# Kernel optimization log

Measured on AMD Instinct MI355X. Metric: run time of the kernel, lower is better.

Reference implementation:

```python
import jax, jax.numpy as jnp
import numpy as np

N = 100000
E = 1600000
D_IN = 128
D_H = 128
D_OUT = 128
LN_EPS = 1e-5
NORM_EPS = 1e-12


def _sage_conv(x, src, dst, Wl, bl, Wr):
    # PyG SAGEConv(mean): out = lin_l(mean_{j in N(i)} x_j) + lin_r(x_i)
    msgs = x[src]                                             # [E, d] gather
    summed = jax.ops.segment_sum(msgs, dst, num_segments=N)   # [N, d]
    cnt = jax.ops.segment_sum(jnp.ones((src.shape[0],), x.dtype), dst, num_segments=N)
    mean = summed / jnp.maximum(cnt, 1.0)[:, None]
    return mean @ Wl + bl + x @ Wr


def _layer_norm(x, g, b):
    mu = jnp.mean(x, axis=-1, keepdims=True)
    var = jnp.mean(jnp.square(x - mu), axis=-1, keepdims=True)
    return (x - mu) * jax.lax.rsqrt(var + LN_EPS) * g + b


def setup_inputs() -> dict:
    key = jax.random.key(0)
    ks = jax.random.split(key, 20)
    x = jax.random.normal(ks[0], (N, D_IN), dtype=jnp.float32)
    edge_index = jax.random.randint(ks[1], (2, E), 0, N, dtype=jnp.int64)
    dims = [(D_IN, D_H), (D_H, D_H), (D_H, D_OUT)]
    inp = {"x": x, "edge_index": edge_index}
    for i, (di, do) in enumerate(dims):
        s = 1.0 / np.sqrt(di)
        inp[f"Wl{i}"] = jax.random.normal(ks[2 + 5 * i], (di, do), dtype=jnp.float32) * s
        inp[f"bl{i}"] = jnp.zeros((do,), dtype=jnp.float32)
        inp[f"Wr{i}"] = jax.random.normal(ks[3 + 5 * i], (di, do), dtype=jnp.float32) * s
        inp[f"g{i}"] = jnp.ones((do,), dtype=jnp.float32)
        inp[f"b{i}"] = jnp.zeros((do,), dtype=jnp.float32)
    return inp


def reference(x, edge_index, Wl0, bl0, Wr0, g0, b0, Wl1, bl1, Wr1, g1, b1, Wl2, bl2, Wr2, g2, b2):
    src, dst = edge_index[0], edge_index[1]
    params = [(Wl0, bl0, Wr0, g0, b0), (Wl1, bl1, Wr1, g1, b1), (Wl2, bl2, Wr2, g2, b2)]
    h = x
    for i, (Wl, bl, Wr, g, b) in enumerate(params):
        h = _sage_conv(h, src, dst, Wl, bl, Wr)
        h = _layer_norm(h, g, b)
        if i < len(params) - 1:
            h = jax.nn.elu(h)
            # dropout is identity in eval mode
    # F.normalize(p=2, dim=-1)
    nrm = jnp.sqrt(jnp.sum(jnp.square(h), axis=-1, keepdims=True))
    return h / jnp.maximum(nrm, NORM_EPS)
```

## Files before the change

### kernel.cpp

```cpp
#include <hip/hip_runtime.h>
#include <hip/hip_bf16.h>
#include <math.h>

#define N_NODES 100000
#define N_EDGES 1600000
#define D 128
#define NB 391
#define BSTRIDE 6000

#define OFF_SSRC 0
#define OFF_OFFS 6400000
#define OFF_PACK 6800016
#define OFF_GC   7193232
#define OFF_BB   7195296
#define OFF_M    7204112
#define OFF_XHI  58404112
#define OFF_XLO  84004112

typedef __attribute__((ext_vector_type(8))) short short8;
typedef __attribute__((ext_vector_type(4))) float floatx4;

__device__ __forceinline__ unsigned short f2bf(float f) {
    unsigned int u = __float_as_uint(f);
    u += 0x7fffu + ((u >> 16) & 1u);
    return (unsigned short)(u >> 16);
}
__device__ __forceinline__ float bf2f(unsigned short h) {
    return __uint_as_float(((unsigned int)h) << 16);
}

__global__ __launch_bounds__(256) void part_kernel(const int* __restrict__ src,
                                                   const int* __restrict__ dst,
                                                   int* __restrict__ gcur,
                                                   uint2* __restrict__ staging) {
    __shared__ int hist[NB];
    __shared__ int base[NB];
    int t = threadIdx.x;
    int e0 = blockIdx.x * 4096;
    for (int i = t; i < NB; i += 256) hist[i] = 0;
    __syncthreads();
    int d[16];
#pragma unroll
    for (int i = 0; i < 16; ++i) {
        int e = e0 + i * 256 + t;
        d[i] = (e < N_EDGES) ? dst[e] : -1;
        if (d[i] >= 0) atomicAdd(&hist[d[i] >> 8], 1);
    }
    __syncthreads();
    for (int i = t; i < NB; i += 256) {
        int h = hist[i];
        base[i] = h ? atomicAdd(&gcur[i], h) : 0;
    }
    __syncthreads();
    for (int i = t; i < NB; i += 256) hist[i] = 0;
    __syncthreads();
#pragma unroll
    for (int i = 0; i < 16; ++i) {
        if (d[i] >= 0) {
            int e = e0 + i * 256 + t;
            int b = d[i] >> 8;
            int slot = atomicAdd(&hist[b], 1);
            staging[b * BSTRIDE + base[b] + slot] =
                make_uint2((unsigned)src[e], (unsigned)(d[i] & 255));
        }
    }
}

__global__ void bscan_kernel(const int* __restrict__ gcur, int* __restrict__ bbase,
                             int* __restrict__ offs) {
    __shared__ int sh[512];
    int t = threadIdx.x;
    int v = (t < NB) ? gcur[t] : 0;
    sh[t] = v;
    __syncthreads();
    for (int off = 1; off < 512; off <<= 1) {
        int y = (t >= off) ? sh[t - off] : 0;
        __syncthreads();
        sh[t] += y;
        __syncthreads();
    }
    if (t < NB) bbase[t] = sh[t] - v;
    if (t == 0) offs[N_NODES] = N_EDGES;
}

__global__ __launch_bounds__(256) void bsort_kernel(const uint2* __restrict__ staging,
                                                    const int* __restrict__ gcur,
                                                    const int* __restrict__ bbase,
                                                    int* __restrict__ offs,
                                                    int* __restrict__ s_src) {
    __shared__ int cnt[256];
    __shared__ int scn[256];
    __shared__ int ssrc[BSTRIDE];
    int b = blockIdx.x;
    int t = threadIdx.x;
    int n = gcur[b];
    int base_out = bbase[b];
    cnt[t] = 0;
    __syncthreads();
    for (int e = t; e < n; e += 256) {
        uint2 v = staging[b * BSTRIDE + e];
        atomicAdd(&cnt[v.y], 1);
    }
    __syncthreads();
    int v = cnt[t];
    scn[t] = v;
    __syncthreads();
    for (int off = 1; off < 256; off <<= 1) {
        int y = (t >= off) ? scn[t - off] : 0;
        __syncthreads();
        scn[t] += y;
        __syncthreads();
    }
    int ex = scn[t] - v;
    int node = b * 256 + t;
    if (node < N_NODES) offs[node] = base_out + ex;
    cnt[t] = ex;
    __syncthreads();
    for (int e = t; e < n; e += 256) {
        uint2 w = staging[b * BSTRIDE + e];
        int slot = atomicAdd(&cnt[w.y], 1);
        ssrc[slot] = (int)w.x;
    }
    __syncthreads();
    for (int e = t; e < n; e += 256) s_src[base_out + e] = ssrc[e];
}

__global__ void pack_kernel(const float* __restrict__ Wl0, const float* __restrict__ Wr0,
                            const float* __restrict__ Wl1, const float* __restrict__ Wr1,
                            const float* __restrict__ Wl2, const float* __restrict__ Wr2,
                            unsigned short* __restrict__ pack) {
    int tid = blockIdx.x * blockDim.x + threadIdx.x;
    int l = tid >> 15;
    int r = tid & 32767;
    int k = r >> 7;
    int n = r & 127;
    const float* Wl = (l == 0) ? Wl0 : (l == 1) ? Wl1 : Wl2;
    const float* Wr = (l == 0) ? Wr0 : (l == 1) ? Wr1 : Wr2;
    float v = (k < 128) ? Wl[k * 128 + n] : Wr[(k - 128) * 128 + n];
    unsigned short hi = f2bf(v);
    unsigned short lo = f2bf(v - bf2f(hi));
    int ct = n >> 4, ks = k >> 5, lane = ((k >> 3) & 3) * 16 + (n & 15), j = k & 7;
    int idx = ((ct * 8 + ks) * 64 + lane) * 8 + j;
    pack[l * 65536 + idx] = hi;
    pack[l * 65536 + 32768 + idx] = lo;
}

__global__ __launch_bounds__(256) void cvt_kernel(const float* __restrict__ x,
                                                  unsigned int* __restrict__ Xhi,
                                                  unsigned int* __restrict__ Xlo) {
    int i = blockIdx.x * 256 + threadIdx.x;
    float2 v = ((const float2*)x)[i];
    unsigned short h0 = f2bf(v.x), h1 = f2bf(v.y);
    unsigned short l0 = f2bf(v.x - bf2f(h0)), l1 = f2bf(v.y - bf2f(h1));
    Xhi[i] = (unsigned int)h0 | ((unsigned int)h1 << 16);
    Xlo[i] = (unsigned int)l0 | ((unsigned int)l1 << 16);
}

__global__ __launch_bounds__(256) void agg_kernel(const uint4* __restrict__ X4,
                                                  const int* __restrict__ s_src,
                                                  const int* __restrict__ offs,
                                                  float* __restrict__ mean) {
    int wid = threadIdx.x >> 6, lane = threadIdx.x & 63;
    int node = blockIdx.x * 4 + wid;
    int sub = lane >> 4, li = lane & 15;
    int beg = offs[node], end = offs[node + 1];
    int deg = end - beg;
    float acc[8];
#pragma unroll
    for (int j = 0; j < 8; ++j) acc[j] = 0.f;

#define ACC_U4(u)                                                                  \
    do {                                                                           \
        const unsigned int w_[4] = {(u).x, (u).y, (u).z, (u).w};                   \
        _Pragma("unroll") for (int j_ = 0; j_ < 4; ++j_) {                         \
            acc[2 * j_]     += bf2f((unsigned short)w_[j_]);                       \
            acc[2 * j_ + 1] += bf2f((unsigned short)(w_[j_] >> 16));               \
        }                                                                          \
    } while (0)

    for (int cbase = 0; cbase < deg; cbase += 64) {
        int cnt = min(deg - cbase, 64);
        int myidx = s_src[min(beg + cbase + lane, N_EDGES - 1)];
        int j = 0;
        for (; j + 16 <= cnt; j += 16) {
            int i0 = __shfl(myidx, j + sub);
            int i1 = __shfl(myidx, j + 4 + sub);
            int i2 = __shfl(myidx, j + 8 + sub);
            int i3 = __shfl(myidx, j + 12 + sub);
            uint4 u0 = X4[i0 * 16 + li];
            uint4 u1 = X4[i1 * 16 + li];
            uint4 u2 = X4[i2 * 16 + li];
            uint4 u3 = X4[i3 * 16 + li];
            ACC_U4(u0);
            ACC_U4(u1);
            ACC_U4(u2);
            ACC_U4(u3);
        }
        if (j + 8 <= cnt) {
            int i0 = __shfl(myidx, j + sub);
            int i1 = __shfl(myidx, j + 4 + sub);
            uint4 u0 = X4[i0 * 16 + li];
            uint4 u1 = X4[i1 * 16 + li];
            ACC_U4(u0);
            ACC_U4(u1);
            j += 8;
        }
        if (j + 4 <= cnt) {
            int i0 = __shfl(myidx, j + sub);
            uint4 u0 = X4[i0 * 16 + li];
            ACC_U4(u0);
            j += 4;
        }
        int rem = cnt - j;
        if (rem > 0) {
            int i0 = __shfl(myidx, j + min(sub, rem - 1));
            uint4 u0 = X4[i0 * 16 + li];
            if (sub < rem) ACC_U4(u0);
        }
    }
#undef ACC_U4

#pragma unroll
    for (int j = 0; j < 8; ++j) {
        acc[j] += __shfl_xor(acc[j], 16);
        acc[j] += __shfl_xor(acc[j], 32);
    }
    float inv = 1.0f / fmaxf((float)deg, 1.0f);
    if (sub < 2) {
        float4 v = make_float4(acc[sub * 4] * inv, acc[sub * 4 + 1] * inv,
                               acc[sub * 4 + 2] * inv, acc[sub * 4 + 3] * inv);
        *(float4*)&mean[node * D + li * 8 + sub * 4] = v;
    }
}

__global__ __launch_bounds__(256) void mmln_kernel(unsigned short* Xh,
                                                   unsigned short* Xl,
                                                   const float* __restrict__ mean,
                                                   const unsigned short* __restrict__ packh,
                                                   const unsigned short* __restrict__ packl,
                                                   const float* __restrict__ bl,
                                                   const float* __restrict__ g,
                                                   const float* __restrict__ b,
                                                   float* __restrict__ outf, int last) {
    int t = threadIdx.x;
    int lane = t & 63;
    int wid = t >> 6;
    int colb = lane & 15;
    int quad = lane >> 4;
    int kq = quad * 8;
    int tilebase = blockIdx.x * 128 + wid * 32;

    int rowA[2];
    rowA[0] = min(tilebase + colb, N_NODES - 1);
    rowA[1] = min(tilebase + 16 + colb, N_NODES - 1);

    floatx4 acc[2][8];
#pragma unroll
    for (int rt = 0; rt < 2; ++rt)
#pragma unroll
        for (int ct = 0; ct < 8; ++ct) acc[rt][ct] = (floatx4){0.f, 0.f, 0.f, 0.f};

#pragma unroll
    for (int ks = 0; ks < 4; ++ks) {
        int kof = ks * 32 + kq;
        short8 ah[2], al[2];
#pragma unroll
        for (int rt = 0; rt < 2; ++rt) {
            const float* p = mean + (long)rowA[rt] * D + kof;
            float4 v0 = *(const float4*)p;
            float4 v1 = *(const float4*)(p + 4);
            float v[8] = {v0.x, v0.y, v0.z, v0.w, v1.x, v1.y, v1.z, v1.w};
#pragma unroll
            for (int j = 0; j < 8; ++j) {
                unsigned short hi = f2bf(v[j]);
                ah[rt][j] = (short)hi;
                al[rt][j] = (short)f2bf(v[j] - bf2f(hi));
            }
        }
#pragma unroll
        for (int ct = 0; ct < 8; ++ct) {
            int fo = ((ct * 8 + ks) << 9) + (lane << 3);
            short8 bh = *(const short8*)(packh + fo);
            short8 bo = *(const short8*)(packl + fo);
#pragma unroll
            for (int rt = 0; rt < 2; ++rt) {
                acc[rt][ct] = __builtin_amdgcn_mfma_f32_16x16x32_bf16(ah[rt], bh, acc[rt][ct], 0, 0, 0);
                acc[rt][ct] = __builtin_amdgcn_mfma_f32_16x16x32_bf16(al[rt], bh, acc[rt][ct], 0, 0, 0);
                acc[rt][ct] = __builtin_amdgcn_mfma_f32_16x16x32_bf16(ah[rt], bo, acc[rt][ct], 0, 0, 0);
            }
        }
    }
#pragma unroll
    for (int ks = 4; ks < 8; ++ks) {
        int kof = (ks - 4) * 32 + kq;
        short8 ah[2], al[2];
#pragma unroll
        for (int rt = 0; rt < 2; ++rt) {
            long o = (long)rowA[rt] * D + kof;
            ah[rt] = *(const short8*)(Xh + o);
            al[rt] = *(const short8*)(Xl + o);
        }
#pragma unroll
        for (int ct = 0; ct < 8; ++ct) {
            int fo = ((ct * 8 + ks) << 9) + (lane << 3);
            short8 bh = *(const short8*)(packh + fo);
            short8 bo = *(const short8*)(packl + fo);
#pragma unroll
            for (int rt = 0; rt < 2; ++rt) {
                acc[rt][ct] = __builtin_amdgcn_mfma_f32_16x16x32_bf16(ah[rt], bh, acc[rt][ct], 0, 0, 0);
                acc[rt][ct] = __builtin_amdgcn_mfma_f32_16x16x32_bf16(al[rt], bh, acc[rt][ct], 0, 0, 0);
                acc[rt][ct] = __builtin_amdgcn_mfma_f32_16x16x32_bf16(ah[rt], bo, acc[rt][ct], 0, 0, 0);
            }
        }
    }

    float bb[8], gg[8], b2[8];
#pragma unroll
    for (int ct = 0; ct < 8; ++ct) {
        bb[ct] = bl[ct * 16 + colb];
        gg[ct] = g[ct * 16 + colb];
        b2[ct] = b[ct * 16 + colb];
    }

#pragma unroll
    for (int rt = 0; rt < 2; ++rt) {
#pragma unroll
        for (int ct = 0; ct < 8; ++ct)
#pragma unroll
            for (int e = 0; e < 4; ++e) acc[rt][ct][e] += bb[ct];
        float mu[4], rstd[4];
#pragma unroll
        for (int e = 0; e < 4; ++e) {
            float s = 0.f;
#pragma unroll
            for (int ct = 0; ct < 8; ++ct) s += acc[rt][ct][e];
            s += __shfl_xor(s, 1); s += __shfl_xor(s, 2);
            s += __shfl_xor(s, 4); s += __shfl_xor(s, 8);
            mu[e] = s * (1.0f / 128.0f);
        }
#pragma unroll
        for (int e = 0; e < 4; ++e) {
            float q = 0.f;
#pragma unroll
            for (int ct = 0; ct < 8; ++ct) {
                float d = acc[rt][ct][e] - mu[e];
                q += d * d;
            }
            q += __shfl_xor(q, 1); q += __shfl_xor(q, 2);
            q += __shfl_xor(q, 4); q += __shfl_xor(q, 8);
            rstd[e] = rsqrtf(q * (1.0f / 128.0f) + 1e-5f);
        }
#pragma unroll
        for (int ct = 0; ct < 8; ++ct)
#pragma unroll
            for (int e = 0; e < 4; ++e) {
                float y = (acc[rt][ct][e] - mu[e]) * rstd[e] * gg[ct] + b2[ct];
                if (!last) y = (y > 0.f) ? y : expm1f(y);
                acc[rt][ct][e] = y;
            }
        if (last) {
#pragma unroll
            for (int e = 0; e < 4; ++e) {
                float ss = 0.f;
#pragma unroll
                for (int ct = 0; ct < 8; ++ct) {
                    float y = acc[rt][ct][e];
                    ss += y * y;
                }
                ss += __shfl_xor(ss, 1); ss += __shfl_xor(ss, 2);
                ss += __shfl_xor(ss, 4); ss += __shfl_xor(ss, 8);
                float inv = 1.0f / fmaxf(sqrtf(ss), 1e-12f);
#pragma unroll
                for (int ct = 0; ct < 8; ++ct) acc[rt][ct][e] *= inv;
            }
#pragma unroll
            for (int e = 0; e < 4; ++e) {
                int row = tilebase + rt * 16 + quad * 4 + e;
                if (row < N_NODES) {
#pragma unroll
                    for (int ct = 0; ct < 8; ++ct)
                        outf[(long)row * D + ct * 16 + colb] = acc[rt][ct][e];
                }
            }
        } else {
#pragma unroll
            for (int e = 0; e < 4; ++e) {
                int row = tilebase + rt * 16 + quad * 4 + e;
                if (row < N_NODES) {
#pragma unroll
                    for (int ct = 0; ct < 8; ++ct) {
                        float y = acc[rt][ct][e];
                        unsigned short hh = f2bf(y);
                        unsigned short ll = f2bf(y - bf2f(hh));
                        long o = (long)row * D + ct * 16 + colb;
                        Xh[o] = hh;
                        Xl[o] = ll;
                    }
                }
            }
        }
    }
}

extern "C" void kernel_launch(void* const* d_in, const int* in_sizes, int n_in,
                              void* d_out, int out_size, void* d_ws, size_t ws_size,
                              hipStream_t stream) {
    const float* x = (const float*)d_in[0];
    const int* edges = (const int*)d_in[1];
    const int* src = edges;
    const int* dst = edges + N_EDGES;
    const float* Wl[3] = {(const float*)d_in[2], (const float*)d_in[7],  (const float*)d_in[12]};
    const float* bl[3] = {(const float*)d_in[3], (const float*)d_in[8],  (const float*)d_in[13]};
    const float* Wr[3] = {(const float*)d_in[4], (const float*)d_in[9],  (const float*)d_in[14]};
    const float* g[3]  = {(const float*)d_in[5], (const float*)d_in[10], (const float*)d_in[15]};
    const float* b[3]  = {(const float*)d_in[6], (const float*)d_in[11], (const float*)d_in[16]};

    char* ws = (char*)d_ws;
    int* s_src = (int*)(ws + OFF_SSRC);
    int* offs  = (int*)(ws + OFF_OFFS);
    unsigned short* wpack = (unsigned short*)(ws + OFF_PACK);
    int* gcur  = (int*)(ws + OFF_GC);
    int* bbase = (int*)(ws + OFF_BB);
    float* M = (float*)(ws + OFF_M);
    uint2* staging = (uint2*)(ws + OFF_M);
    unsigned short* Xhi = (unsigned short*)(ws + OFF_XHI);
    unsigned short* Xlo = (unsigned short*)(ws + OFF_XLO);
    float* out = (float*)d_out;

    hipMemsetAsync(gcur, 0, NB * sizeof(int), stream);
    part_kernel<<<(N_EDGES + 4095) / 4096, 256, 0, stream>>>(src, dst, gcur, staging);
    bscan_kernel<<<1, 512, 0, stream>>>(gcur, bbase, offs);
    bsort_kernel<<<NB, 256, 0, stream>>>(staging, gcur, bbase, offs, s_src);
    pack_kernel<<<(3 * 32768) / 256, 256, 0, stream>>>(Wl[0], Wr[0], Wl[1], Wr[1], Wl[2], Wr[2], wpack);
    cvt_kernel<<<(N_NODES * 64) / 256, 256, 0, stream>>>(x, (unsigned int*)Xhi, (unsigned int*)Xlo);

    const int MMB = (N_NODES + 127) / 128;
    unsigned short* ph[3] = {wpack, wpack + 65536, wpack + 131072};

    agg_kernel<<<N_NODES / 4, 256, 0, stream>>>((const uint4*)Xhi, s_src, offs, M);
    mmln_kernel<<<MMB, 256, 0, stream>>>(Xhi, Xlo, M, ph[0], ph[0] + 32768, bl[0], g[0], b[0], nullptr, 0);
    agg_kernel<<<N_NODES / 4, 256, 0, stream>>>((const uint4*)Xhi, s_src, offs, M);
    mmln_kernel<<<MMB, 256, 0, stream>>>(Xhi, Xlo, M, ph[1], ph[1] + 32768, bl[1], g[1], b[1], nullptr, 0);
    agg_kernel<<<N_NODES / 4, 256, 0, stream>>>((const uint4*)Xhi, s_src, offs, M);
    mmln_kernel<<<MMB, 256, 0, stream>>>(Xhi, Xlo, M, ph[2], ph[2] + 32768, bl[2], g[2], b[2], out, 1);
}
```

Baseline: 638.6 us.

## Fuse neighbor mean aggregation with matmul+LayerNorm via LDS, ping-pong feature buffers

Result: slower. 720.0 us (+12.8%).

```diff
diff --git a/kernel.cpp b/kernel.cpp
--- a/kernel.cpp
+++ b/kernel.cpp
@@ -16,6 +16,8 @@
 #define OFF_M    7204112
 #define OFF_XHI  58404112
 #define OFF_XLO  84004112
+
+#define LSTRIDE 130
 
 typedef __attribute__((ext_vector_type(8))) short short8;
 typedef __attribute__((ext_vector_type(4))) float floatx4;
@@ -156,18 +158,26 @@
     Xlo[i] = (unsigned int)l0 | ((unsigned int)l1 << 16);
 }
 
-__global__ __launch_bounds__(256) void agg_kernel(const uint4* __restrict__ X4,
-                                                  const int* __restrict__ s_src,
-                                                  const int* __restrict__ offs,
-                                                  float* __restrict__ mean) {
-    int wid = threadIdx.x >> 6, lane = threadIdx.x & 63;
-    int node = blockIdx.x * 4 + wid;
+__global__ __launch_bounds__(128) void fused_kernel(const uint4* __restrict__ X4,
+                                                    const unsigned short* __restrict__ Xh,
+                                                    const unsigned short* __restrict__ Xl,
+                                                    unsigned short* __restrict__ XhO,
+                                                    unsigned short* __restrict__ XlO,
+                                                    const int* __restrict__ s_src,
+                                                    const int* __restrict__ offs,
+                                                    const unsigned short* __restrict__ packh,
+                                                    const unsigned short* __restrict__ packl,
+                                                    const float* __restrict__ bl,
+                                                    const float* __restrict__ g,
+                                                    const float* __restrict__ b,
+                                                    float* __restrict__ outf, int last) {
+    __shared__ float lmean[64 * LSTRIDE];
+    int t = threadIdx.x;
+    int wid = t >> 6, lane = t & 63;
     int sub = lane >> 4, li = lane & 15;
-    int beg = offs[node], end = offs[node + 1];
-    int deg = end - beg;
-    float acc[8];
-#pragma unroll
-    for (int j = 0; j < 8; ++j) acc[j] = 0.f;
+    int nodebase = blockIdx.x * 64;
+
+    int off_l = offs[min(nodebase + wid * 32 + min(lane, 32), N_NODES)];
 
 #define ACC_U4(u)                                                                  \
     do {                                                                           \
@@ -178,81 +188,76 @@
         }                                                                          \
     } while (0)
 
-    for (int cbase = 0; cbase < deg; cbase += 64) {
-        int cnt = min(deg - cbase, 64);
-        int myidx = s_src[min(beg + cbase + lane, N_EDGES - 1)];
-        int j = 0;
-        for (; j + 16 <= cnt; j += 16) {
-            int i0 = __shfl(myidx, j + sub);
-            int i1 = __shfl(myidx, j + 4 + sub);
-            int i2 = __shfl(myidx, j + 8 + sub);
-            int i3 = __shfl(myidx, j + 12 + sub);
-            uint4 u0 = X4[i0 * 16 + li];
-            uint4 u1 = X4[i1 * 16 + li];
-            uint4 u2 = X4[i2 * 16 + li];
-            uint4 u3 = X4[i3 * 16 + li];
-            ACC_U4(u0);
-            ACC_U4(u1);
-            ACC_U4(u2);
-            ACC_U4(u3);
-        }
-        if (j + 8 <= cnt) {
-            int i0 = __shfl(myidx, j + sub);
-            int i1 = __shfl(myidx, j + 4 + sub);
-            uint4 u0 = X4[i0 * 16 + li];
-            uint4 u1 = X4[i1 * 16 + li];
-            ACC_U4(u0);
-            ACC_U4(u1);
-            j += 8;
-        }
-        if (j + 4 <= cnt) {
-            int i0 = __shfl(myidx, j + sub);
-            uint4 u0 = X4[i0 * 16 + li];
-            ACC_U4(u0);
-            j += 4;
-        }
-        int rem = cnt - j;
-        if (rem > 0) {
-            int i0 = __shfl(myidx, j + min(sub, rem - 1));
-            uint4 u0 = X4[i0 * 16 + li];
-            if (sub < rem) ACC_U4(u0);
+    for (int i = 0; i < 32; ++i) {
+        int lrow = wid * 32 + i;
+        int beg = __shfl(off_l, i);
+        int end = __shfl(off_l, i + 1);
+        int deg = end - beg;
+        float acc[8];
+#pragma unroll
+        for (int j = 0; j < 8; ++j) acc[j] = 0.f;
+
+        for (int cbase = 0; cbase < deg; cbase += 64) {
+            int cnt = min(deg - cbase, 64);
+            int myidx = s_src[min(beg + cbase + lane, N_EDGES - 1)];
+            int j = 0;
+            for (; j + 16 <= cnt; j += 16) {
+                int i0 = __shfl(myidx, j + sub);
+                int i1 = __shfl(myidx, j + 4 + sub);
+                int i2 = __shfl(myidx, j + 8 + sub);
+                int i3 = __shfl(myidx, j + 12 + sub);
+                uint4 u0 = X4[i0 * 16 + li];
+                uint4 u1 = X4[i1 * 16 + li];
+                uint4 u2 = X4[i2 * 16 + li];
+                uint4 u3 = X4[i3 * 16 + li];
+                ACC_U4(u0); ACC_U4(u1); ACC_U4(u2); ACC_U4(u3);
+            }
+            if (j + 8 <= cnt) {
+                int i0 = __shfl(myidx, j + sub);
+                int i1 = __shfl(myidx, j + 4 + sub);
+                uint4 u0 = X4[i0 * 16 + li];
+                uint4 u1 = X4[i1 * 16 + li];
+                ACC_U4(u0); ACC_U4(u1);
+                j += 8;
+            }
+            if (j + 4 <= cnt) {
+                int i0 = __shfl(myidx, j + sub);
+                uint4 u0 = X4[i0 * 16 + li];
+                ACC_U4(u0);
+                j += 4;
+            }
+            int rem = cnt - j;
+            if (rem > 0) {
+                int i0 = __shfl(myidx, j + min(sub, rem - 1));
+                uint4 u0 = X4[i0 * 16 + li];
+                if (sub < rem) ACC_U4(u0);
+            }
+        }
+#pragma unroll
+        for (int j = 0; j < 8; ++j) {
+            acc[j] += __shfl_xor(acc[j], 16);
+            acc[j] += __shfl_xor(acc[j], 32);
+        }
+        float inv = 1.0f / fmaxf((float)deg, 1.0f);
+        if (sub < 2) {
+            floatx4 v = {acc[sub * 4] * inv, acc[sub * 4 + 1] * inv,
+                         acc[sub * 4 + 2] * inv, acc[sub * 4 + 3] * inv};
+            *(floatx4*)&lmean[lrow * LSTRIDE + li * 8 + sub * 4] = v;
         }
     }
 #undef ACC_U4
-
-#pragma unroll
-    for (int j = 0; j < 8; ++j) {
-        acc[j] += __shfl_xor(acc[j], 16);
-        acc[j] += __shfl_xor(acc[j], 32);
-    }
-    float inv = 1.0f / fmaxf((float)deg, 1.0f);
-    if (sub < 2) {
-        float4 v = make_float4(acc[sub * 4] * inv, acc[sub * 4 + 1] * inv,
-                               acc[sub * 4 + 2] * inv, acc[sub * 4 + 3] * inv);
-        *(float4*)&mean[node * D + li * 8 + sub * 4] = v;
-    }
-}
-
-__global__ __launch_bounds__(256) void mmln_kernel(unsigned short* Xh,
-                                                   unsigned short* Xl,
-                                                   const float* __restrict__ mean,
-                                                   const unsigned short* __restrict__ packh,
-                                                   const unsigned short* __restrict__ packl,
-                                                   const float* __restrict__ bl,
-                                                   const float* __restrict__ g,
-                                                   const float* __restrict__ b,
-                                                   float* __restrict__ outf, int last) {
-    int t = threadIdx.x;
-    int lane = t & 63;
-    int wid = t >> 6;
+    __syncthreads();
+
     int colb = lane & 15;
     int quad = lane >> 4;
     int kq = quad * 8;
-    int tilebase = blockIdx.x * 128 + wid * 32;
-
-    int rowA[2];
+    int tilebase = nodebase + wid * 32;
+
+    int rowA[2], lrowA[2];
     rowA[0] = min(tilebase + colb, N_NODES - 1);
     rowA[1] = min(tilebase + 16 + colb, N_NODES - 1);
+    lrowA[0] = wid * 32 + colb;
+    lrowA[1] = wid * 32 + 16 + colb;
 
     floatx4 acc[2][8];
 #pragma unroll
@@ -266,10 +271,10 @@
         short8 ah[2], al[2];
 #pragma unroll
         for (int rt = 0; rt < 2; ++rt) {
-            const float* p = mean + (long)rowA[rt] * D + kof;
-            float4 v0 = *(const float4*)p;
-            float4 v1 = *(const float4*)(p + 4);
-            float v[8] = {v0.x, v0.y, v0.z, v0.w, v1.x, v1.y, v1.z, v1.w};
+            const float* p = &lmean[lrowA[rt] * LSTRIDE + kof];
+            floatx4 v0 = *(const floatx4*)p;
+            floatx4 v1 = *(const floatx4*)(p + 4);
+            float v[8] = {v0[0], v0[1], v0[2], v0[3], v1[0], v1[1], v1[2], v1[3]};
 #pragma unroll
             for (int j = 0; j < 8; ++j) {
                 unsigned short hi = f2bf(v[j]);
@@ -393,8 +398,8 @@
                         unsigned short hh = f2bf(y);
                         unsigned short ll = f2bf(y - bf2f(hh));
                         long o = (long)row * D + ct * 16 + colb;
-                        Xh[o] = hh;
-                        Xl[o] = ll;
+                        XhO[o] = hh;
+                        XlO[o] = ll;
                     }
                 }
             }
@@ -421,10 +426,11 @@
     unsigned short* wpack = (unsigned short*)(ws + OFF_PACK);
     int* gcur  = (int*)(ws + OFF_GC);
     int* bbase = (int*)(ws + OFF_BB);
-    float* M = (float*)(ws + OFF_M);
     uint2* staging = (uint2*)(ws + OFF_M);
-    unsigned short* Xhi = (unsigned short*)(ws + OFF_XHI);
-    unsigned short* Xlo = (unsigned short*)(ws + OFF_XLO);
+    unsigned short* XhB = (unsigned short*)(ws + OFF_M);
+    unsigned short* XlB = (unsigned short*)(ws + OFF_M + 25600000);
+    unsigned short* XhA = (unsigned short*)(ws + OFF_XHI);
+    unsigned short* XlA = (unsigned short*)(ws + OFF_XLO);
     float* out = (float*)d_out;
 
     hipMemsetAsync(gcur, 0, NB * sizeof(int), stream);
@@ -432,15 +438,18 @@
     bscan_kernel<<<1, 512, 0, stream>>>(gcur, bbase, offs);
     bsort_kernel<<<NB, 256, 0, stream>>>(staging, gcur, bbase, offs, s_src);
     pack_kernel<<<(3 * 32768) / 256, 256, 0, stream>>>(Wl[0], Wr[0], Wl[1], Wr[1], Wl[2], Wr[2], wpack);
-    cvt_kernel<<<(N_NODES * 64) / 256, 256, 0, stream>>>(x, (unsigned int*)Xhi, (unsigned int*)Xlo);
-
-    const int MMB = (N_NODES + 127) / 128;
+    cvt_kernel<<<(N_NODES * 64) / 256, 256, 0, stream>>>(x, (unsigned int*)XhA, (unsigned int*)XlA);
+
+    const int FB = (N_NODES + 63) / 64;
     unsigned short* ph[3] = {wpack, wpack + 65536, wpack + 131072};
 
-    agg_kernel<<<N_NODES / 4, 256, 0, stream>>>((const uint4*)Xhi, s_src, offs, M);
-    mmln_kernel<<<MMB, 256, 0, stream>>>(Xhi, Xlo, M, ph[0], ph[0] + 32768, bl[0], g[0], b[0], nullptr, 0);
-    agg_kernel<<<N_NODES / 4, 256, 0, stream>>>((const uint4*)Xhi, s_src, offs, M);
-    mmln_kernel<<<MMB, 256, 0, stream>>>(Xhi, Xlo, M, ph[1], ph[1] + 32768, bl[1], g[1], b[1], nullptr, 0);
-    agg_kernel<<<N_NODES / 4, 256, 0, stream>>>((const uint4*)Xhi, s_src, offs, M);
-    mmln_kernel<<<MMB, 256, 0, stream>>>(Xhi, Xlo, M, ph[2], ph[2] + 32768, bl[2], g[2], b[2], out, 1);
-}
+    fused_kernel<<<FB, 128, 0, stream>>>((const uint4*)XhA, XhA, XlA, XhB, XlB,
+                                         s_src, offs, ph[0], ph[0] + 32768,
+                                         bl[0], g[0], b[0], nullptr, 0);
+    fused_kernel<<<FB, 128, 0, stream>>>((const uint4*)XhB, XhB, XlB, XhA, XlA,
+                                         s_src, offs, ph[1], ph[1] + 32768,
+                                         bl[1], g[1], b[1], nullptr, 0);
+    fused_kernel<<<FB, 128, 0, stream>>>((const uint4*)XhA, XhA, XlA, nullptr, nullptr,
+                                         s_src, offs, ph[2], ph[2] + 32768,
+                                         bl[2], g[2], b[2], out, 1);
+}
```
